# Performance work log

Measured on AMD Instinct MI355X. Metric: run time of the kernel, lower is better.

Reference implementation:

```python
import jax, jax.numpy as jnp
import numpy as np

B, N, C = 4, 4096, 256
H = W = 512
PATCH = 4
MIN_PATCH = 4
POS_MAX = 124  # ensures pos*MIN_PATCH + PATCH - 1 < W


def setup_inputs() -> dict:
    key = jax.random.key(0)
    k1, k2, k3, k4 = jax.random.split(key, 4)
    feat = jax.random.normal(k1, (B, N, C), dtype=jnp.float32)
    images = jax.random.uniform(k2, (B, 3, H, W), dtype=jnp.float32)
    pos_org = jax.random.randint(k3, (B, N, 2), 0, POS_MAX).astype(jnp.int32)
    # shuffled positions: per-batch permutation of pos_org (as produced by the backbone's token shuffle)
    perm = jax.vmap(lambda k: jax.random.permutation(k, N))(jax.random.split(k4, B))
    pos_shuffled = jnp.take_along_axis(pos_org, perm[..., None], axis=1)
    return {"feat": feat, "images": images, "pos_org": pos_org,
            "pos_shuffled": pos_shuffled, "patch_size": PATCH, "min_patch_size": MIN_PATCH}


def _compute_color_dist(im):
    # edge map: sum of L1 color distances to 4-neighbors (symmetric, so each pair added once per side)
    def cd(a, b):
        return jnp.abs(a[:, 0] - b[:, 0]) + jnp.abs(a[:, 1] - b[:, 1]) + jnp.abs(a[:, 2] - b[:, 2])
    Bm, _, Hm, Wm = im.shape
    em = jnp.zeros((Bm, Hm, Wm), im.dtype)
    dv = cd(im[:, :, 1:, :], im[:, :, :-1, :])
    em = em.at[:, 1:, :].add(dv)
    em = em.at[:, :-1, :].add(dv)
    dh = cd(im[:, :, :, 1:], im[:, :, :, :-1])
    em = em.at[:, :, 1:].add(dh)
    em = em.at[:, :, :-1].add(dh)
    return em


def reference(feat, images, pos_org, pos_shuffled, patch_size, min_patch_size):
    # --- find_pos_org_order: brute-force 1-NN (L1 cdist + argmin) ---
    d = jnp.sum(jnp.abs(pos_org[:, :, None, :].astype(jnp.float32)
                        - pos_shuffled[:, None, :, :].astype(jnp.float32)), axis=-1)  # [B,N,N]
    idx = jnp.argmin(d, axis=2)                                    # [B,N]
    # --- gather-based reorder: feat[b_, pos_indices] ---
    feat_r = jnp.take_along_axis(feat, idx[..., None], axis=1)     # [B,N,C]
    # --- generate_color_change_upsampling_mask (vectorized over batch) ---
    em = _compute_color_dist(images)                               # [B,H,W]
    p_org = pos_org * min_patch_size                               # pixel coords [B,N,2]
    pc = jnp.stack(jnp.meshgrid(jnp.arange(patch_size), jnp.arange(patch_size),
                                indexing='ij'), axis=-1).reshape(-1, 2)  # [P*P,2]
    pp = p_org[:, :, None, :] + pc[None, None]                     # [B,N,P*P,2]
    x, y = pp[..., 0], pp[..., 1]
    vals = em[jnp.arange(em.shape[0])[:, None, None], y, x]        # [B,N,P*P] irregular gather
    dis = vals.sum(-1)                                             # [B,N] disagreement map
    return feat_r, dis
```

## Files before the change

kernel.cpp:

```cpp
#include <hip/hip_runtime.h>
#include <cstdint>
#include <cstddef>

#define BATCH 4
#define NTOK  4096
#define CCH   256
#define IMH   512
#define IMW   512

#define RPB 8
#define NBLOCKS (BATCH * NTOK / RPB)

typedef float v4f __attribute__((ext_vector_type(4)));

__device__ __forceinline__ float dis48(const float* __restrict__ im,
                                       int b, int key, int lane) {
    float s = 0.f;
    if (lane < 48) {
        const int px  = key >> 16;
        const int py  = key & 0xFFFF;
        const int ch  = lane >> 4;
        const int k   = lane & 15;
        const int col = px * 4 + (k >> 2);
        const int r   = py * 4 + (k & 3);
        const float* base = im + (((size_t)(b * 3 + ch)) * IMH + r) * IMW + col;
        const bool up = (r > 0), dn = (r < IMH - 1);
        const bool lf = (col > 0), rt = (col < IMW - 1);
        const float vC = base[0];
        const float vU = base[up ? -IMW : 0];
        const float vD = base[dn ?  IMW : 0];
        const float vL = base[lf ?   -1 : 0];
        const float vR = base[rt ?    1 : 0];
        s  = up ? fabsf(vC - vU) : 0.f;
        s += dn ? fabsf(vD - vC) : 0.f;
        s += lf ? fabsf(vC - vL) : 0.f;
        s += rt ? fabsf(vR - vC) : 0.f;
    }
    return s;
}

__global__ __launch_bounds__(256) void fused_k(const float4* __restrict__ feat,
                                               const float* __restrict__ im,
                                               const int2* __restrict__ po,
                                               const int4* __restrict__ ps4,
                                               float4* __restrict__ out_feat,
                                               float* __restrict__ out_dis) {
    __shared__ int s_key[RPB];
    __shared__ int s_idx[RPB];

    const int tid = threadIdx.x;
    const int r0  = blockIdx.x * RPB;
    const int b   = r0 >> 12;

    if (tid < RPB) {
        int2 p = po[r0 + tid];
        s_key[tid] = (p.x << 16) | p.y;
        s_idx[tid] = 0x7FFFFFFF;
    }
    __syncthreads();

    int kreg[RPB];
#pragma unroll
    for (int k = 0; k < RPB; ++k) kreg[k] = s_key[k];

    const int4* psb = ps4 + (size_t)b * (NTOK / 2);
    int4 t[8];
#pragma unroll
    for (int it = 0; it < 8; ++it) t[it] = psb[it * 256 + tid];

#pragma unroll
    for (int it = 0; it < 8; ++it) {
        const int e0 = (t[it].x << 16) | t[it].y;
        const int e1 = (t[it].z << 16) | t[it].w;
        const int j0 = 2 * (it * 256 + tid);
#pragma unroll
        for (int k = 0; k < RPB; ++k) {
            if (e0 == kreg[k]) atomicMin(&s_idx[k], j0);
            if (e1 == kreg[k]) atomicMin(&s_idx[k], j0 + 1);
        }
    }
    __syncthreads();

    const int lane = tid & 63;
    const int w    = tid >> 6;
    const int li0  = w * 2, li1 = w * 2 + 1;
    const int row0 = r0 + li0, row1 = r0 + li1;
    const int idx0 = s_idx[li0], idx1 = s_idx[li1];
    const int key0 = s_key[li0], key1 = s_key[li1];

    const float4 f0 = feat[((size_t)(b * NTOK + idx0)) * 64 + lane];
    const float4 f1 = feat[((size_t)(b * NTOK + idx1)) * 64 + lane];

    float s0 = dis48(im, b, key0, lane);
    float s1 = dis48(im, b, key1, lane);

    v4f n0 = { f0.x, f0.y, f0.z, f0.w };
    v4f n1 = { f1.x, f1.y, f1.z, f1.w };
    __builtin_nontemporal_store(n0, (v4f*)&out_feat[(size_t)row0 * 64 + lane]);
    __builtin_nontemporal_store(n1, (v4f*)&out_feat[(size_t)row1 * 64 + lane]);

#pragma unroll
    for (int d = 1; d < 64; d <<= 1) s0 += __shfl_xor(s0, d, 64);
#pragma unroll
    for (int d = 1; d < 64; d <<= 1) s1 += __shfl_xor(s1, d, 64);
    if (lane == 0) {
        __builtin_nontemporal_store(s0, &out_dis[row0]);
        __builtin_nontemporal_store(s1, &out_dis[row1]);
    }
}

extern "C" void kernel_launch(void* const* d_in, const int* in_sizes, int n_in,
                              void* d_out, int out_size, void* d_ws, size_t ws_size,
                              hipStream_t stream) {
    const float* feat         = (const float*)d_in[0];
    const float* images       = (const float*)d_in[1];
    const int*   pos_org      = (const int*)d_in[2];
    const int*   pos_shuffled = (const int*)d_in[3];

    float* out_feat = (float*)d_out;
    float* out_dis  = out_feat + (size_t)BATCH * NTOK * CCH;

    fused_k<<<NBLOCKS, 256, 0, stream>>>(
        (const float4*)feat, images, (const int2*)pos_org,
        (const int4*)pos_shuffled, (float4*)out_feat, out_dis);
}
```

Baseline: 19.95 us.

## Double rows per block, vectorize edge-map loads and prefetch them before NN search

Raises rows per block from 8 to 16, halving the block count and the number of times each block rescans the full shuffled-position array. The disagreement computation now assigns one 16-lane group per row and loads each patch row as a float4 plus left and right scalars, using the in-patch symmetric horizontal differences instead of five scalar loads per pixel. These image loads are issued before the nearest-neighbor matching loop so their latency overlaps the atomic search. The cost is more registers and more shared-memory atomics per block, and it relies on the patch never touching the bottom or right image border.

After: 21.13 us. +5.9%, slower.

```diff
diff --git a/kernel.cpp b/kernel.cpp
--- a/kernel.cpp
+++ b/kernel.cpp
@@ -8,36 +8,10 @@
 #define IMH   512
 #define IMW   512
 
-#define RPB 8
+#define RPB 16
 #define NBLOCKS (BATCH * NTOK / RPB)
 
 typedef float v4f __attribute__((ext_vector_type(4)));
-
-__device__ __forceinline__ float dis48(const float* __restrict__ im,
-                                       int b, int key, int lane) {
-    float s = 0.f;
-    if (lane < 48) {
-        const int px  = key >> 16;
-        const int py  = key & 0xFFFF;
-        const int ch  = lane >> 4;
-        const int k   = lane & 15;
-        const int col = px * 4 + (k >> 2);
-        const int r   = py * 4 + (k & 3);
-        const float* base = im + (((size_t)(b * 3 + ch)) * IMH + r) * IMW + col;
-        const bool up = (r > 0), dn = (r < IMH - 1);
-        const bool lf = (col > 0), rt = (col < IMW - 1);
-        const float vC = base[0];
-        const float vU = base[up ? -IMW : 0];
-        const float vD = base[dn ?  IMW : 0];
-        const float vL = base[lf ?   -1 : 0];
-        const float vR = base[rt ?    1 : 0];
-        s  = up ? fabsf(vC - vU) : 0.f;
-        s += dn ? fabsf(vD - vC) : 0.f;
-        s += lf ? fabsf(vC - vL) : 0.f;
-        s += rt ? fabsf(vR - vC) : 0.f;
-    }
-    return s;
-}
 
 __global__ __launch_bounds__(256) void fused_k(const float4* __restrict__ feat,
                                                const float* __restrict__ im,
@@ -50,7 +24,7 @@
 
     const int tid = threadIdx.x;
     const int r0  = blockIdx.x * RPB;
-    const int b   = r0 >> 12;
+    const int b   = blockIdx.x >> 8;
 
     if (tid < RPB) {
         int2 p = po[r0 + tid];
@@ -58,6 +32,31 @@
         s_idx[tid] = 0x7FFFFFFF;
     }
     __syncthreads();
+
+    const int lane = tid & 63;
+    const int w    = tid >> 6;
+
+    const int q    = lane >> 4;
+    const int unit = lane & 15;
+    const int drow = r0 + w * 4 + q;
+    const int dkey = s_key[w * 4 + q];
+    const bool act = unit < 12;
+
+    const int px = dkey >> 16, py = dkey & 0xFFFF;
+    const int ch = unit >> 2,  pr = unit & 3;
+    const int rimg = py * 4 + pr;
+    const int col0 = px * 4;
+    const float* dbase = im + (((size_t)(b * 3 + ch)) * IMH + rimg) * IMW + col0;
+
+    v4f vC = {0,0,0,0}, vU = {0,0,0,0}, vD = {0,0,0,0};
+    float vL = 0.f, vR = 0.f;
+    if (act) {
+        vC = *(const v4f*)dbase;
+        vU = *(const v4f*)(rimg > 0 ? dbase - IMW : dbase);
+        vD = *(const v4f*)(dbase + IMW);
+        vL = (col0 > 0) ? dbase[-1] : 0.f;
+        vR = dbase[4];
+    }
 
     int kreg[RPB];
 #pragma unroll
@@ -81,32 +80,34 @@
     }
     __syncthreads();
 
-    const int lane = tid & 63;
-    const int w    = tid >> 6;
-    const int li0  = w * 2, li1 = w * 2 + 1;
-    const int row0 = r0 + li0, row1 = r0 + li1;
-    const int idx0 = s_idx[li0], idx1 = s_idx[li1];
-    const int key0 = s_key[li0], key1 = s_key[li1];
+#pragma unroll
+    for (int qq = 0; qq < 4; ++qq) {
+        const int row = r0 + w * 4 + qq;
+        const int idx = s_idx[w * 4 + qq];
+        const float4 f = feat[((size_t)(b * NTOK + idx)) * 64 + lane];
+        v4f n = { f.x, f.y, f.z, f.w };
+        __builtin_nontemporal_store(n, (v4f*)&out_feat[(size_t)row * 64 + lane]);
+    }
 
-    const float4 f0 = feat[((size_t)(b * NTOK + idx0)) * 64 + lane];
-    const float4 f1 = feat[((size_t)(b * NTOK + idx1)) * 64 + lane];
-
-    float s0 = dis48(im, b, key0, lane);
-    float s1 = dis48(im, b, key1, lane);
-
-    v4f n0 = { f0.x, f0.y, f0.z, f0.w };
-    v4f n1 = { f1.x, f1.y, f1.z, f1.w };
-    __builtin_nontemporal_store(n0, (v4f*)&out_feat[(size_t)row0 * 64 + lane]);
-    __builtin_nontemporal_store(n1, (v4f*)&out_feat[(size_t)row1 * 64 + lane]);
-
-#pragma unroll
-    for (int d = 1; d < 64; d <<= 1) s0 += __shfl_xor(s0, d, 64);
-#pragma unroll
-    for (int d = 1; d < 64; d <<= 1) s1 += __shfl_xor(s1, d, 64);
-    if (lane == 0) {
-        __builtin_nontemporal_store(s0, &out_dis[row0]);
-        __builtin_nontemporal_store(s1, &out_dis[row1]);
+    float s = 0.f;
+    if (act) {
+        const float su = fabsf(vC.x - vU.x) + fabsf(vC.y - vU.y)
+                       + fabsf(vC.z - vU.z) + fabsf(vC.w - vU.w);
+        if (rimg > 0) s += su;
+        s += fabsf(vD.x - vC.x) + fabsf(vD.y - vC.y)
+           + fabsf(vD.z - vC.z) + fabsf(vD.w - vC.w);
+        const float d01 = fabsf(vC.y - vC.x);
+        const float d12 = fabsf(vC.z - vC.y);
+        const float d23 = fabsf(vC.w - vC.z);
+        s += 2.f * (d01 + d12 + d23);
+        if (col0 > 0) s += fabsf(vC.x - vL);
+        s += fabsf(vR - vC.w);
     }
+    s += __shfl_xor(s, 1, 16);
+    s += __shfl_xor(s, 2, 16);
+    s += __shfl_xor(s, 4, 16);
+    s += __shfl_xor(s, 8, 16);
+    if (unit == 0) __builtin_nontemporal_store(s, &out_dis[drow]);
 }
 
 extern "C" void kernel_launch(void* const* d_in, const int* in_sizes, int n_in,
```
